# Performance work log

Measured on AMD Instinct MI355X. Metric: run time of the kernel, lower is better.

The kernel has to match this reference:

```python
import jax, jax.numpy as jnp
import numpy as np

BN_EPS = 1e-5


def setup_inputs() -> dict:
    key = jax.random.key(0)
    ks = jax.random.split(key, 6)
    N, C, T, V = 64, 64, 300, 25
    num_A, O = 3, 64
    x = jax.random.normal(ks[0], (N, C, T, V), dtype=jnp.float32)
    A = jax.random.uniform(ks[1], (num_A, V, V), dtype=jnp.float32)
    # 1x1 conv weights per adjacency branch: W[a, o, c], bias b[a, o]
    W = jax.random.normal(ks[2], (num_A, O, C), dtype=jnp.float32) * (1.0 / np.sqrt(C))
    b = jax.random.normal(ks[3], (num_A, O), dtype=jnp.float32) * 0.01
    gamma = jnp.ones((O,), dtype=jnp.float32)
    beta = jnp.zeros((O,), dtype=jnp.float32)
    return {"x": x, "A": A, "W": W, "b": b, "gamma": gamma, "beta": beta}


def reference(x, A, W, b, gamma, beta):
    # x: [N, C, T, V]; A: [num_A, V, V]; W: [num_A, O, C]; b: [num_A, O]
    # For each branch a: xa = x @ A_a over the joint dim V, then a 1x1 conv
    # (channel mix W_a + bias b_a), accumulated over branches.
    z = jnp.einsum('nctv,avw->anctw', x, A)          # [num_A, N, C, T, V]
    y = jnp.einsum('anctw,aoc->notw', z, W)          # [N, O, T, V]
    y = y + jnp.sum(b, axis=0)[None, :, None, None]
    # BatchNorm2d (training mode: batch statistics over N, T, V per channel)
    mean = jnp.mean(y, axis=(0, 2, 3), keepdims=True)
    var = jnp.mean((y - mean) ** 2, axis=(0, 2, 3), keepdims=True)
    y = (y - mean) * jax.lax.rsqrt(var + BN_EPS)
    y = y * gamma[None, :, None, None] + beta[None, :, None, None]
    return jax.nn.relu(y)
```

## Files before the change

### kernel.cpp

```cpp
#include <hip/hip_runtime.h>


typedef __attribute__((ext_vector_type(8))) short short8;
typedef __attribute__((ext_vector_type(4))) float f32x4;

static __device__ __forceinline__ float bf2f(unsigned short u) {
    return __uint_as_float(((unsigned)u) << 16);
}
static __device__ __forceinline__ unsigned short f2bf(float f) {
    unsigned u = __float_as_uint(f);
    u += 0x7FFFu + ((u >> 16) & 1u);
    return (unsigned short)(u >> 16);
}
static __device__ __forceinline__ unsigned pack2bf(float a, float b) {
    return (unsigned)f2bf(a) | ((unsigned)f2bf(b) << 16);
}

#define MFMA16(a, b, c) __builtin_amdgcn_mfma_f32_16x16x32_bf16((a), (b), (c), 0, 0, 0)

#define ZSTRIDE 72

__global__ __launch_bounds__(256, 4)
void gcn_k1(const void* __restrict__ xg, const void* __restrict__ Ag,
            const void* __restrict__ Wg, const void* __restrict__ gammag,
            float* __restrict__ gstats, unsigned short* __restrict__ y_ws)
{
    const int tid  = threadIdx.x;
    const int wv   = tid >> 6;
    const int lane = tid & 63;
    const int n16  = lane & 15;
    const int kg   = lane >> 4;
    const int bx   = blockIdx.x;
    const int nb   = bx / 75;
    const int tile = bx - nb * 75;

    const bool isbf = (*(const unsigned*)gammag) == 0x3F803F80u;

    __shared__ __align__(16) unsigned short xs2[256 * 32];
    __shared__ __align__(16) unsigned short AsT[3 * 32 * 32];
    __shared__ __align__(16) unsigned short zsT[112 * ZSTRIDE];
    __shared__ float red[128];

    if (tid < 128) red[tid] = 0.f;
    for (int s = tid; s < 12 * ZSTRIDE; s += 256) zsT[100 * ZSTRIDE + s] = 0;

    short8 wfrag[3][2];
    #pragma unroll
    for (int a = 0; a < 3; ++a)
        #pragma unroll
        for (int k2 = 0; k2 < 2; ++k2) {
            const int off = (a * 64 + wv * 16 + n16) * 64 + k2 * 32 + kg * 8;
            if (isbf) {
                wfrag[a][k2] = *(const short8*)((const unsigned short*)Wg + off);
            } else {
                const float* wp = (const float*)Wg + off;
                const float4 w0 = *(const float4*)wp;
                const float4 w1 = *(const float4*)(wp + 4);
                short8 f;
                f[0] = (short)f2bf(w0.x); f[1] = (short)f2bf(w0.y);
                f[2] = (short)f2bf(w0.z); f[3] = (short)f2bf(w0.w);
                f[4] = (short)f2bf(w1.x); f[5] = (short)f2bf(w1.y);
                f[6] = (short)f2bf(w1.z); f[7] = (short)f2bf(w1.w);
                wfrag[a][k2] = f;
            }
        }

    for (int s = tid; s < 3072; s += 256) {
        const int a = s >> 10, w = (s >> 5) & 31, v = s & 31;
        unsigned short val = 0;
        if (v < 25 && w < 25) {
            const int src = (a * 25 + v) * 25 + w;
            val = isbf ? ((const unsigned short*)Ag)[src] : f2bf(((const float*)Ag)[src]);
        }
        AsT[s] = val;
    }

    {
        #pragma unroll
        for (int vv = 25; vv < 32; ++vv) xs2[tid * 32 + vv] = 0;
    }
    if (isbf) {
        const unsigned* xp = (const unsigned*)xg;
        for (int p = tid; p < 3200; p += 256) {
            const int c = p / 50, pc = p - c * 50;
            const unsigned u = xp[(nb * 64 + c) * 3750 + tile * 50 + pc];
            const int r0 = pc * 2, r1 = r0 + 1;
            const int dt0 = r0 / 25, v0 = r0 - dt0 * 25;
            const int dt1 = r1 / 25, v1 = r1 - dt1 * 25;
            xs2[(dt0 * 64 + c) * 32 + v0] = (unsigned short)(u & 0xFFFFu);
            xs2[(dt1 * 64 + c) * 32 + v1] = (unsigned short)(u >> 16);
        }
    } else {
        const float2* xp = (const float2*)xg;
        for (int p = tid; p < 3200; p += 256) {
            const int c = p / 50, pc = p - c * 50;
            const float2 f = xp[(nb * 64 + c) * 3750 + tile * 50 + pc];
            const int r0 = pc * 2, r1 = r0 + 1;
            const int dt0 = r0 / 25, v0 = r0 - dt0 * 25;
            const int dt1 = r1 / 25, v1 = r1 - dt1 * 25;
            xs2[(dt0 * 64 + c) * 32 + v0] = f2bf(f.x);
            xs2[(dt1 * 64 + c) * 32 + v1] = f2bf(f.y);
        }
    }

    __syncthreads();

    short8 af[4];
    #pragma unroll
    for (int mt = 0; mt < 4; ++mt)
        af[mt] = *(const short8*)&xs2[(wv * 64 + mt * 16 + n16) * 32 + kg * 8];

    f32x4 acc[7];
    const f32x4 zero4 = (f32x4){0.f, 0.f, 0.f, 0.f};
    #pragma unroll
    for (int mt = 0; mt < 7; ++mt) acc[mt] = zero4;

    #pragma unroll
    for (int a = 0; a < 3; ++a) {
        const short8 bA0 = *(const short8*)&AsT[(a * 32 +      n16) * 32 + kg * 8];
        const short8 bA1 = *(const short8*)&AsT[(a * 32 + 16 + n16) * 32 + kg * 8];
        #pragma unroll
        for (int mt = 0; mt < 4; ++mt) {
            const f32x4 d0 = MFMA16(af[mt], bA0, zero4);
            const f32x4 d1 = MFMA16(af[mt], bA1, zero4);
            const int h = mt * 16 + kg * 4;
            *(uint2*)&zsT[(wv * 25 + n16) * ZSTRIDE + h] =
                make_uint2(pack2bf(d0[0], d0[1]), pack2bf(d0[2], d0[3]));
            if (n16 < 9)
                *(uint2*)&zsT[(wv * 25 + 16 + n16) * ZSTRIDE + h] =
                    make_uint2(pack2bf(d1[0], d1[1]), pack2bf(d1[2], d1[3]));
        }
        __syncthreads();

        #pragma unroll
        for (int mt = 0; mt < 7; ++mt) {
            #pragma unroll
            for (int k2 = 0; k2 < 2; ++k2) {
                const short8 bf = *(const short8*)&zsT[(mt * 16 + n16) * ZSTRIDE
                                                       + k2 * 32 + kg * 8];
                acc[mt] = MFMA16(wfrag[a][k2], bf, acc[mt]);
            }
        }
        __syncthreads();
    }

    #pragma unroll
    for (int r = 0; r < 4; ++r) {
        const int o = 16 * wv + kg * 4 + r;
        const unsigned rowbase = (unsigned)(nb * 64 + o) * 7500u + (unsigned)tile * 100u;
        float s = 0.f, q = 0.f;
        #pragma unroll
        for (int mt = 0; mt < 7; ++mt) {
            const float v = acc[mt][r];
            const bool valid = (mt < 6) | (n16 < 4);
            const float vm = valid ? v : 0.f;
            s += vm; q += vm * vm;
            const float vhi = __shfl_xor(v, 1);
            if (((n16 & 1) == 0) && valid)
                *(unsigned*)(y_ws + rowbase + (unsigned)(mt * 16 + n16)) = pack2bf(v, vhi);
        }
        #pragma unroll
        for (int off = 1; off < 16; off <<= 1) {
            s += __shfl_xor(s, off);
            q += __shfl_xor(q, off);
        }
        if (n16 == 0) { atomicAdd(&red[o], s); atomicAdd(&red[64 + o], q); }
    }

    __syncthreads();
    if (tid < 128) atomicAdd(&gstats[tid], red[tid]);
}

__global__ __launch_bounds__(256)
void gcn_k2(const float* __restrict__ gstats, const unsigned* __restrict__ y32,
            const void* __restrict__ gammag, const void* __restrict__ betag,
            void* __restrict__ outg)
{
    __shared__ float sc[64], sh[64];
    const int tid = threadIdx.x;
    const bool isbf = (*(const unsigned*)gammag) == 0x3F803F80u;

    if (tid < 64) {
        const float inv  = 1.0f / 480000.0f;
        const float mean = gstats[tid] * inv;
        const float var  = gstats[64 + tid] * inv - mean * mean;
        const float rstd = rsqrtf(var + 1e-5f);
        float g, be;
        if (isbf) { g = bf2f(((const unsigned short*)gammag)[tid]); be = bf2f(((const unsigned short*)betag)[tid]); }
        else      { g = ((const float*)gammag)[tid];                be = ((const float*)betag)[tid]; }
        sc[tid] = g * rstd;
        sh[tid] = be - mean * g * rstd;
    }
    __syncthreads();

    const unsigned i = blockIdx.x * 256u + (unsigned)tid;
    const uint4 u = ((const uint4*)y32)[i];
    const unsigned b = i * 4u;
    unsigned wv[4] = {u.x, u.y, u.z, u.w};
    float res[8];
    #pragma unroll
    for (int j = 0; j < 4; ++j) {
        const unsigned o = ((b + j) / 3750u) & 63u;
        const float scl = sc[o], shf = sh[o];
        const float v0 = bf2f((unsigned short)(wv[j] & 0xFFFFu));
        const float v1 = bf2f((unsigned short)(wv[j] >> 16));
        res[2 * j]     = fmaxf(fmaf(v0, scl, shf), 0.f);
        res[2 * j + 1] = fmaxf(fmaf(v1, scl, shf), 0.f);
    }
    if (isbf) {
        uint4 outp;
        outp.x = (unsigned)f2bf(res[0]) | ((unsigned)f2bf(res[1]) << 16);
        outp.y = (unsigned)f2bf(res[2]) | ((unsigned)f2bf(res[3]) << 16);
        outp.z = (unsigned)f2bf(res[4]) | ((unsigned)f2bf(res[5]) << 16);
        outp.w = (unsigned)f2bf(res[6]) | ((unsigned)f2bf(res[7]) << 16);
        ((uint4*)outg)[i] = outp;
    } else {
        float4 f0 = make_float4(res[0], res[1], res[2], res[3]);
        float4 f1 = make_float4(res[4], res[5], res[6], res[7]);
        ((float4*)outg)[2 * i]     = f0;
        ((float4*)outg)[2 * i + 1] = f1;
    }
}

extern "C" void kernel_launch(void* const* d_in, const int* in_sizes, int n_in,
                              void* d_out, int out_size, void* d_ws, size_t ws_size,
                              hipStream_t stream)
{
    (void)in_sizes; (void)n_in; (void)out_size; (void)ws_size;
    const void* x     = d_in[0];
    const void* A     = d_in[1];
    const void* W     = d_in[2];
    const void* gamma = d_in[4];
    const void* beta  = d_in[5];

    float*          gstats = (float*)d_ws;
    unsigned short* y_ws   = (unsigned short*)d_ws + 256;

    hipMemsetAsync(d_ws, 0, 512, stream);
    gcn_k1<<<dim3(64 * 75), dim3(256), 0, stream>>>(x, A, W, gamma, gstats, y_ws);
    gcn_k2<<<dim3(15000), dim3(256), 0, stream>>>(gstats, (const unsigned*)y_ws, gamma, beta, d_out);
}
```

Before: 377.3 us.

## Alias x and z LDS buffers, raise occupancy, and spread stats atomics across slots

Shares one LDS pool between the staged x tile and the z intermediate, adding a barrier once the x fragments are in registers, so per-block shared memory shrinks and the launch bound rises to 6 blocks per CU. The final per-block atomics for the BatchNorm sums are spread over 64 slot arrays instead of one 128-float array, and a new single-block kernel reduces the slots. The aim is less contention on the global atomics and better latency hiding. In exchange it adds an extra kernel launch, a larger memset, and more register pressure under the tighter launch bound.

Result: faster. 327.0 us (-13.3%).

```diff
diff --git a/kernel.cpp b/kernel.cpp
--- a/kernel.cpp
+++ b/kernel.cpp
@@ -19,11 +19,12 @@
 #define MFMA16(a, b, c) __builtin_amdgcn_mfma_f32_16x16x32_bf16((a), (b), (c), 0, 0, 0)
 
 #define ZSTRIDE 72
-
-__global__ __launch_bounds__(256, 4)
+#define NSLOT   64
+
+__global__ __launch_bounds__(256, 6)
 void gcn_k1(const void* __restrict__ xg, const void* __restrict__ Ag,
             const void* __restrict__ Wg, const void* __restrict__ gammag,
-            float* __restrict__ gstats, unsigned short* __restrict__ y_ws)
+            float* __restrict__ pslots, unsigned short* __restrict__ y_ws)
 {
     const int tid  = threadIdx.x;
     const int wv   = tid >> 6;
@@ -36,13 +37,13 @@
 
     const bool isbf = (*(const unsigned*)gammag) == 0x3F803F80u;
 
-    __shared__ __align__(16) unsigned short xs2[256 * 32];
+    __shared__ __align__(16) char pool[16384];
+    unsigned short* const xs2 = (unsigned short*)pool;
+    unsigned short* const zsT = (unsigned short*)pool;
     __shared__ __align__(16) unsigned short AsT[3 * 32 * 32];
-    __shared__ __align__(16) unsigned short zsT[112 * ZSTRIDE];
     __shared__ float red[128];
 
     if (tid < 128) red[tid] = 0.f;
-    for (int s = tid; s < 12 * ZSTRIDE; s += 256) zsT[100 * ZSTRIDE + s] = 0;
 
     short8 wfrag[3][2];
     #pragma unroll
@@ -110,6 +111,11 @@
     for (int mt = 0; mt < 4; ++mt)
         af[mt] = *(const short8*)&xs2[(wv * 64 + mt * 16 + n16) * 32 + kg * 8];
 
+    __syncthreads();
+
+    for (int s = tid; s < 432; s += 256)
+        ((unsigned*)(zsT + 100 * ZSTRIDE))[s] = 0;
+
     f32x4 acc[7];
     const f32x4 zero4 = (f32x4){0.f, 0.f, 0.f, 0.f};
     #pragma unroll
@@ -141,7 +147,7 @@
                 acc[mt] = MFMA16(wfrag[a][k2], bf, acc[mt]);
             }
         }
-        __syncthreads();
+        if (a < 2) __syncthreads();
     }
 
     #pragma unroll
@@ -168,11 +174,22 @@
     }
 
     __syncthreads();
-    if (tid < 128) atomicAdd(&gstats[tid], red[tid]);
+    if (tid < 128) atomicAdd(&pslots[(bx & (NSLOT - 1)) * 128 + tid], red[tid]);
+}
+
+__global__ __launch_bounds__(128)
+void gcn_kred(const float* __restrict__ pslots, float* __restrict__ gfin)
+{
+    const int t = threadIdx.x;
+    float s = 0.f;
+    #pragma unroll
+    for (int sl = 0; sl < NSLOT; ++sl)
+        s += pslots[sl * 128 + t];
+    gfin[t] = s;
 }
 
 __global__ __launch_bounds__(256)
-void gcn_k2(const float* __restrict__ gstats, const unsigned* __restrict__ y32,
+void gcn_k2(const float* __restrict__ gfin, const unsigned* __restrict__ y32,
             const void* __restrict__ gammag, const void* __restrict__ betag,
             void* __restrict__ outg)
 {
@@ -182,8 +199,8 @@
 
     if (tid < 64) {
         const float inv  = 1.0f / 480000.0f;
-        const float mean = gstats[tid] * inv;
-        const float var  = gstats[64 + tid] * inv - mean * mean;
+        const float mean = gfin[tid] * inv;
+        const float var  = gfin[64 + tid] * inv - mean * mean;
         const float rstd = rsqrtf(var + 1e-5f);
         float g, be;
         if (isbf) { g = bf2f(((const unsigned short*)gammag)[tid]); be = bf2f(((const unsigned short*)betag)[tid]); }
@@ -233,10 +250,12 @@
     const void* gamma = d_in[4];
     const void* beta  = d_in[5];
 
-    float*          gstats = (float*)d_ws;
-    unsigned short* y_ws   = (unsigned short*)d_ws + 256;
-
-    hipMemsetAsync(d_ws, 0, 512, stream);
-    gcn_k1<<<dim3(64 * 75), dim3(256), 0, stream>>>(x, A, W, gamma, gstats, y_ws);
-    gcn_k2<<<dim3(15000), dim3(256), 0, stream>>>(gstats, (const unsigned*)y_ws, gamma, beta, d_out);
-}
+    float*          pslots = (float*)d_ws;
+    float*          gfin   = (float*)((char*)d_ws + 32768);
+    unsigned short* y_ws   = (unsigned short*)((char*)d_ws + 33280);
+
+    hipMemsetAsync(d_ws, 0, 32768, stream);
+    gcn_k1<<<dim3(64 * 75), dim3(256), 0, stream>>>(x, A, W, gamma, pslots, y_ws);
+    gcn_kred<<<dim3(1), dim3(128), 0, stream>>>(pslots, gfin);
+    gcn_k2<<<dim3(15000), dim3(256), 0, stream>>>(gfin, (const unsigned*)y_ws, gamma, beta, d_out);
+}
```
